# Optimization experiments

Hardware: AMD Instinct MI355X
Metric: run time of the kernel (lower is better)

Reference implementation:

```python
import jax, jax.numpy as jnp
import numpy as np

M, K1, N1, N2, N3 = 131072, 256, 1024, 1024, 256


def setup_inputs() -> dict:
    key = jax.random.key(0)
    k_x, k1, k2, k3 = jax.random.split(key, 4)
    x = jax.random.normal(k_x, (M, K1), dtype=jnp.float32)
    # Kaiming-ish scaling so softplus stays in a sane range
    w1 = jax.random.normal(k1, (K1, N1), dtype=jnp.float32) * (1.0 / np.sqrt(K1))
    w2 = jax.random.normal(k2, (N1, N2), dtype=jnp.float32) * (1.0 / np.sqrt(N1))
    w3 = jax.random.normal(k3, (N2, N3), dtype=jnp.float32) * (1.0 / np.sqrt(N2))
    return {"x": x, "w1": w1, "w2": w2, "w3": w3}


def reference(x, w1, w2, w3):
    # Fused 3-layer MLP: out = softplus(softplus(x @ W1) @ W2) @ W3
    h1 = jax.nn.softplus(x @ w1)   # [M, N1]
    h2 = jax.nn.softplus(h1 @ w2)  # [M, N2]
    return h2 @ w3                 # [M, N3]
```

## Files before the change

### kernel.cpp

```cpp
#include <hip/hip_runtime.h>

typedef __attribute__((ext_vector_type(8))) short short8;
typedef __attribute__((ext_vector_type(4))) float floatx4;
typedef __attribute__((ext_vector_type(2))) unsigned int uintx2;
typedef __attribute__((ext_vector_type(4))) unsigned int uintx4;
typedef unsigned short u16;

#define MFMA(a, b, c) __builtin_amdgcn_mfma_f32_16x16x32_bf16((a), (b), (c), 0, 0, 0)
#define BAR() do { asm volatile("" ::: "memory"); __builtin_amdgcn_s_barrier(); \
                   asm volatile("" ::: "memory"); } while (0)
#define LGKM0() asm volatile("s_waitcnt lgkmcnt(0)" ::: "memory")

__device__ __forceinline__ u16 f2bf(float f) {
  unsigned int u = __builtin_bit_cast(unsigned int, f);
  u += ((u >> 16) & 1u) + 0x7fffu;
  return (u16)(u >> 16);
}

__device__ __forceinline__ float softplus_f(float v) {
  float a = __builtin_fabsf(v);
  float e = __expf(-a);
  float l = __logf(1.0f + e);
  return __builtin_fmaxf(v, 0.0f) + l;
}

__device__ __forceinline__ unsigned int pack_sp(float lo, float hi) {
  return (unsigned int)f2bf(softplus_f(lo)) | ((unsigned int)f2bf(softplus_f(hi)) << 16);
}

__global__ void transpose_cvt(const float* __restrict__ in, u16* __restrict__ out, int K, int N) {
  __shared__ float tile[32][33];
  const int bn = blockIdx.x * 32, bk = blockIdx.y * 32;
  const int tx = threadIdx.x, ty = threadIdx.y;
#pragma unroll
  for (int i = 0; i < 32; i += 8)
    tile[ty + i][tx] = in[(size_t)(bk + ty + i) * N + bn + tx];
  __syncthreads();
#pragma unroll
  for (int i = 0; i < 32; i += 8)
    out[(size_t)(bn + ty + i) * K + bk + tx] = f2bf(tile[tx][ty + i]);
}

__device__ __forceinline__ void gld16(const void* g, void* l) {
  __builtin_amdgcn_global_load_lds((const __attribute__((address_space(1))) void*)g,
                                   (__attribute__((address_space(3))) void*)l, 16, 0, 0);
}

template <int LN>
__device__ __forceinline__ void vwait() {
  if constexpr (LN == 0) asm volatile("s_waitcnt vmcnt(0)" ::: "memory");
  else if constexpr (LN == 2) asm volatile("s_waitcnt vmcnt(2)" ::: "memory");
  else if constexpr (LN == 3) asm volatile("s_waitcnt vmcnt(3)" ::: "memory");
}

template <int K, int EPI, bool ACTF32>
__global__ __launch_bounds__(512, 4) void gemm2b(const void* __restrict__ actv,
                                                 const u16* __restrict__ wt,
                                                 void* __restrict__ Cout, int N, int nbn) {
  constexpr int H = K / 32;
  constexpr int BUF = 12288;
  __shared__ u16 lds[2 * BUF];
  u16* L = lds;
  const int tid = threadIdx.x, lane = tid & 63, wv = tid >> 6;
  const int l15 = lane & 15, g = lane >> 4;
  const int wvm = wv >> 2, wvn = wv & 3;
  const int nwg = gridDim.x, o = blockIdx.x;
  const int sw = (o & 7) * (nwg >> 3) + (o >> 3);
  const int bm = sw / nbn, bn = sw % nbn;
  const size_t am0 = (size_t)bm * 128;
  const size_t wn0 = (size_t)bn * 256;

  int afo[4], wfo[4];
#pragma unroll
  for (int mt = 0; mt < 4; ++mt) {
    const int r = wvm * 64 + mt * 16 + l15;
    afo[mt] = (r * 4 + (g ^ ((r >> 1) & 3))) * 8;
  }
#pragma unroll
  for (int nt = 0; nt < 4; ++nt) {
    const int r = wvn * 64 + nt * 16 + l15;
    wfo[nt] = 4096 + (r * 4 + (g ^ ((r >> 1) & 3))) * 8;
  }

  const int rA = tid >> 2, gA = (tid & 3) ^ ((rA >> 1) & 3);
  const int rW1 = 128 + rA, gW1 = (tid & 3) ^ ((rW1 >> 1) & 3);
  const u16* asrc = nullptr;
  const float* fsrc = nullptr;
  if constexpr (ACTF32) fsrc = (const float*)actv + (am0 + rA) * K + gA * 8;
  else asrc = (const u16*)actv + (am0 + rA) * K + gA * 8;
  const u16* wsrc0 = wt + (wn0 + rA) * K + gA * 8;
  const u16* wsrc1 = wt + (wn0 + rW1) * K + gW1 * 8;
  const int dA = tid * 8, dW0 = 4096 + tid * 8, dW1 = 4096 + (512 + tid) * 8;

#define STG_W(hh)                                                       \
  { gld16(wsrc0 + (hh) * 32, L + ((hh) & 1) * BUF + dW0);               \
    gld16(wsrc1 + (hh) * 32, L + ((hh) & 1) * BUF + dW1); }
#define STG_AB(hh) { gld16(asrc + (hh) * 32, L + ((hh) & 1) * BUF + dA); }
#define STG_AF(hh)                                                      \
  { floatx4 v0 = *(const floatx4*)(fsrc + (hh) * 32);                   \
    floatx4 v1 = *(const floatx4*)(fsrc + (hh) * 32 + 4);               \
    uintx4 w_;                                                          \
    w_.x = (unsigned)f2bf(v0.x) | ((unsigned)f2bf(v0.y) << 16);         \
    w_.y = (unsigned)f2bf(v0.z) | ((unsigned)f2bf(v0.w) << 16);         \
    w_.z = (unsigned)f2bf(v1.x) | ((unsigned)f2bf(v1.y) << 16);         \
    w_.w = (unsigned)f2bf(v1.z) | ((unsigned)f2bf(v1.w) << 16);         \
    *(uintx4*)(L + ((hh) & 1) * BUF + dA) = w_; }

  floatx4 acc[4][4];
  const floatx4 z4 = {0.f, 0.f, 0.f, 0.f};
#pragma unroll
  for (int nt = 0; nt < 4; ++nt)
#pragma unroll
    for (int mt = 0; mt < 4; ++mt) acc[nt][mt] = z4;

  if constexpr (ACTF32) { STG_AF(0) STG_W(0) }
  else { STG_AB(0) STG_W(0) }

#pragma unroll 1
  for (int h = 0; h < H; ++h) {
    const int cb = (h & 1) * BUF;
    if (h + 1 < H) {
      if constexpr (ACTF32) { STG_AF(h + 1) STG_W(h + 1) LGKM0(); vwait<2>(); }
      else { STG_AB(h + 1) STG_W(h + 1) vwait<3>(); }
    } else {
      if constexpr (ACTF32) LGKM0();
      vwait<0>();
    }
    BAR();
    short8 af0 = *(const short8*)(L + cb + afo[0]);
    short8 af1 = *(const short8*)(L + cb + afo[1]);
    short8 af2 = *(const short8*)(L + cb + afo[2]);
    short8 af3 = *(const short8*)(L + cb + afo[3]);
    short8 wf0 = *(const short8*)(L + cb + wfo[0]);
    short8 wf1 = *(const short8*)(L + cb + wfo[1]);
    short8 wf2 = *(const short8*)(L + cb + wfo[2]);
    short8 wf3 = *(const short8*)(L + cb + wfo[3]);
    __builtin_amdgcn_s_setprio(1);
    acc[0][0] = MFMA(wf0, af0, acc[0][0]);
    acc[0][1] = MFMA(wf0, af1, acc[0][1]);
    acc[0][2] = MFMA(wf0, af2, acc[0][2]);
    acc[0][3] = MFMA(wf0, af3, acc[0][3]);
    acc[1][0] = MFMA(wf1, af0, acc[1][0]);
    acc[1][1] = MFMA(wf1, af1, acc[1][1]);
    acc[1][2] = MFMA(wf1, af2, acc[1][2]);
    acc[1][3] = MFMA(wf1, af3, acc[1][3]);
    acc[2][0] = MFMA(wf2, af0, acc[2][0]);
    acc[2][1] = MFMA(wf2, af1, acc[2][1]);
    acc[2][2] = MFMA(wf2, af2, acc[2][2]);
    acc[2][3] = MFMA(wf2, af3, acc[2][3]);
    acc[3][0] = MFMA(wf3, af0, acc[3][0]);
    acc[3][1] = MFMA(wf3, af1, acc[3][1]);
    acc[3][2] = MFMA(wf3, af2, acc[3][2]);
    acc[3][3] = MFMA(wf3, af3, acc[3][3]);
    __builtin_amdgcn_s_setprio(0);
    BAR();
  }
#undef STG_W
#undef STG_AB
#undef STG_AF

  __syncthreads();

  if constexpr (EPI == 0) {
    u16* cl = L;
#pragma unroll
    for (int q = 0; q < 2; ++q) {
      if (q) __syncthreads();
      if (wvm == q) {
#pragma unroll
        for (int nt = 0; nt < 4; ++nt)
#pragma unroll
          for (int mt = 0; mt < 4; ++mt) {
            const int m = mt * 16 + l15;
            const int n0 = wvn * 64 + nt * 16 + g * 4;
            const int j = n0 >> 3, hh = (n0 >> 2) & 1;
            uintx2 pk;
            pk.x = pack_sp(acc[nt][mt].x, acc[nt][mt].y);
            pk.y = pack_sp(acc[nt][mt].z, acc[nt][mt].w);
            *(uintx2*)(cl + m * 256 + ((j ^ (m & 7)) << 3) + (hh << 2)) = pk;
          }
      }
      __syncthreads();
      u16* outp = (u16*)Cout;
#pragma unroll
      for (int i = 0; i < 4; ++i) {
        const int c = i * 512 + tid;
        const int m = c >> 5, j = c & 31;
        uintx4 v = *(const uintx4*)(cl + m * 256 + ((j ^ (m & 7)) << 3));
        *(uintx4*)(outp + (am0 + q * 64 + m) * N + wn0 + j * 8) = v;
      }
    }
  } else {
    float* cf = (float*)L;
#pragma unroll
    for (int q = 0; q < 4; ++q) {
      if (q) __syncthreads();
      if (wvm == (q >> 1)) {
#pragma unroll
        for (int nt = 0; nt < 4; ++nt)
#pragma unroll
          for (int mt2 = 0; mt2 < 2; ++mt2) {
            const int mt = (q & 1) * 2 + mt2;
            const int m = mt2 * 16 + l15;
            const int p = (wvn * 64 + nt * 16 + g * 4) >> 1;
            *(floatx4*)(cf + m * 256 + ((p ^ ((m & 7) << 1)) << 1)) = acc[nt][mt];
          }
      }
      __syncthreads();
      float* outp = (float*)Cout;
#pragma unroll
      for (int i = 0; i < 4; ++i) {
        const int c = i * 512 + tid;
        const int m = c >> 6, cc = c & 63;
        const int p = cc * 2;
        floatx4 v = *(const floatx4*)(cf + m * 256 + ((p ^ ((m & 7) << 1)) << 1));
        *(floatx4*)(outp + (am0 + q * 32 + m) * N + wn0 + cc * 4) = v;
      }
    }
  }
}

__global__ __launch_bounds__(512, 2) void mlp3_fused(const float* __restrict__ x,
                                                     const u16* __restrict__ w1t,
                                                     const u16* __restrict__ w2t,
                                                     const u16* __restrict__ w3t,
                                                     float* __restrict__ out) {
  __shared__ u16 h1s[64 * 1024];
  __shared__ u16 xs[64 * 256];
  const int tid = threadIdx.x, lane = tid & 63, wv = tid >> 6;
  const int l15 = lane & 15, g = lane >> 4;
  const size_t m0 = (size_t)blockIdx.x * 64;
  const floatx4 z4 = {0.f, 0.f, 0.f, 0.f};
  {
    const float* xp = x + m0 * 256;
#pragma unroll
    for (int r = 0; r < 8; ++r) {
      int idx4 = r * 512 + tid;
      int m = idx4 >> 6, k = (idx4 & 63) << 2;
      floatx4 v = *(const floatx4*)(xp + m * 256 + k);
      uintx2 pk;
      pk.x = (unsigned)f2bf(v.x) | ((unsigned)f2bf(v.y) << 16);
      pk.y = (unsigned)f2bf(v.z) | ((unsigned)f2bf(v.w) << 16);
      *(uintx2*)(xs + ((m * 256 + k) ^ ((m & 7) << 3))) = pk;
    }
  }
  __syncthreads();
#pragma unroll 1
  for (int c = 0; c < 4; ++c) {
    floatx4 acc[2][4];
#pragma unroll
    for (int t = 0; t < 2; ++t)
#pragma unroll
      for (int mt = 0; mt < 4; ++mt) acc[t][mt] = z4;
    const u16* p0 = w1t + (size_t)(c * 256 + wv * 32 + l15) * 256;
#pragma unroll
    for (int ks = 0; ks < 8; ++ks) {
      const int k = ks * 32 + g * 8;
      short8 a0 = *(const short8*)(p0 + k);
      short8 a1 = *(const short8*)(p0 + 16 * 256 + k);
      short8 b0 = *(const short8*)(xs + (((0 * 16 + l15) * 256 + k) ^ ((l15 & 7) << 3)));
      short8 b1 = *(const short8*)(xs + (((1 * 16 + l15) * 256 + k) ^ ((l15 & 7) << 3)));
      short8 b2 = *(const short8*)(xs + (((2 * 16 + l15) * 256 + k) ^ ((l15 & 7) << 3)));
      short8 b3 = *(const short8*)(xs + (((3 * 16 + l15) * 256 + k) ^ ((l15 & 7) << 3)));
      acc[0][0] = MFMA(a0, b0, acc[0][0]); acc[0][1] = MFMA(a0, b1, acc[0][1]);
      acc[0][2] = MFMA(a0, b2, acc[0][2]); acc[0][3] = MFMA(a0, b3, acc[0][3]);
      acc[1][0] = MFMA(a1, b0, acc[1][0]); acc[1][1] = MFMA(a1, b1, acc[1][1]);
      acc[1][2] = MFMA(a1, b2, acc[1][2]); acc[1][3] = MFMA(a1, b3, acc[1][3]);
    }
#pragma unroll
    for (int t = 0; t < 2; ++t)
#pragma unroll
      for (int mt = 0; mt < 4; ++mt) {
        const int n1 = c * 256 + wv * 32 + t * 16 + g * 4;
        const int m = mt * 16 + l15;
        uintx2 pk;
        pk.x = pack_sp(acc[t][mt].x, acc[t][mt].y);
        pk.y = pack_sp(acc[t][mt].z, acc[t][mt].w);
        *(uintx2*)(h1s + ((m * 1024 + n1) ^ ((m & 7) << 3))) = pk;
      }
  }
  __syncthreads();
  floatx4 acc3[2][4];
#pragma unroll
  for (int t = 0; t < 2; ++t)
#pragma unroll
    for (int mt = 0; mt < 4; ++mt) acc3[t][mt] = z4;
#pragma unroll 1
  for (int c2 = 0; c2 < 4; ++c2) {
    floatx4 acc2[2][4];
#pragma unroll
    for (int t = 0; t < 2; ++t)
#pragma unroll
      for (int mt = 0; mt < 4; ++mt) acc2[t][mt] = z4;
    {
      const u16* p0 = w2t + (size_t)(c2 * 256 + wv * 32 + l15) * 1024;
#pragma unroll 4
      for (int ks = 0; ks < 32; ++ks) {
        const int k = ks * 32 + g * 8;
        short8 a0 = *(const short8*)(p0 + k);
        short8 a1 = *(const short8*)(p0 + 16 * 1024 + k);
        short8 b0 = *(const short8*)(h1s + (((0 * 16 + l15) * 1024 + k) ^ ((l15 & 7) << 3)));
        short8 b1 = *(const short8*)(h1s + (((1 * 16 + l15) * 1024 + k) ^ ((l15 & 7) << 3)));
        short8 b2 = *(const short8*)(h1s + (((2 * 16 + l15) * 1024 + k) ^ ((l15 & 7) << 3)));
        short8 b3 = *(const short8*)(h1s + (((3 * 16 + l15) * 1024 + k) ^ ((l15 & 7) << 3)));
        acc2[0][0] = MFMA(a0, b0, acc2[0][0]); acc2[0][1] = MFMA(a0, b1, acc2[0][1]);
        acc2[0][2] = MFMA(a0, b2, acc2[0][2]); acc2[0][3] = MFMA(a0, b3, acc2[0][3]);
        acc2[1][0] = MFMA(a1, b0, acc2[1][0]); acc2[1][1] = MFMA(a1, b1, acc2[1][1]);
        acc2[1][2] = MFMA(a1, b2, acc2[1][2]); acc2[1][3] = MFMA(a1, b3, acc2[1][3]);
      }
    }
    __syncthreads();
#pragma unroll
    for (int t = 0; t < 2; ++t)
#pragma unroll
      for (int mt = 0; mt < 4; ++mt) {
        const int n2l = wv * 32 + t * 16 + g * 4;
        const int m = mt * 16 + l15;
        uintx2 pk;
        pk.x = pack_sp(acc2[t][mt].x, acc2[t][mt].y);
        pk.y = pack_sp(acc2[t][mt].z, acc2[t][mt].w);
        *(uintx2*)(xs + ((m * 256 + n2l) ^ ((m & 7) << 3))) = pk;
      }
    __syncthreads();
    {
      const u16* p0 = w3t + (size_t)(wv * 32 + l15) * 1024 + c2 * 256;
#pragma unroll
      for (int ks = 0; ks < 8; ++ks) {
        const int k = ks * 32 + g * 8;
        short8 a0 = *(const short8*)(p0 + k);
        short8 a1 = *(const short8*)(p0 + 16 * 1024 + k);
        short8 b0 = *(const short8*)(xs + (((0 * 16 + l15) * 256 + k) ^ ((l15 & 7) << 3)));
        short8 b1 = *(const short8*)(xs + (((1 * 16 + l15) * 256 + k) ^ ((l15 & 7) << 3)));
        short8 b2 = *(const short8*)(xs + (((2 * 16 + l15) * 256 + k) ^ ((l15 & 7) << 3)));
        short8 b3 = *(const short8*)(xs + (((3 * 16 + l15) * 256 + k) ^ ((l15 & 7) << 3)));
        acc3[0][0] = MFMA(a0, b0, acc3[0][0]); acc3[0][1] = MFMA(a0, b1, acc3[0][1]);
        acc3[0][2] = MFMA(a0, b2, acc3[0][2]); acc3[0][3] = MFMA(a0, b3, acc3[0][3]);
        acc3[1][0] = MFMA(a1, b0, acc3[1][0]); acc3[1][1] = MFMA(a1, b1, acc3[1][1]);
        acc3[1][2] = MFMA(a1, b2, acc3[1][2]); acc3[1][3] = MFMA(a1, b3, acc3[1][3]);
      }
    }
  }
#pragma unroll
  for (int t = 0; t < 2; ++t)
#pragma unroll
    for (int mt = 0; mt < 4; ++mt) {
      const int n3 = wv * 32 + t * 16 + g * 4;
      const int m = mt * 16 + l15;
      *(floatx4*)(out + (m0 + m) * 256 + n3) = acc3[t][mt];
    }
}

extern "C" void kernel_launch(void* const* d_in, const int* in_sizes, int n_in,
                              void* d_out, int out_size, void* d_ws, size_t ws_size,
                              hipStream_t stream) {
  const float* x = (const float*)d_in[0];
  const float* w1 = (const float*)d_in[1];
  const float* w2 = (const float*)d_in[2];
  const float* w3 = (const float*)d_in[3];
  float* out = (float*)d_out;
  const size_t M = 131072;

  u16* w1t = (u16*)d_ws;
  u16* w2t = w1t + 1024 * 256;
  u16* w3t = w2t + 1024 * 1024;
  u16* bufA = w3t + 256 * 1024;
  const size_t weights_el = 1024 * 256 + 1024 * 1024 + 256 * 1024;

  size_t CM = 0;
  const size_t cands[4] = {32768, 16384, 8192, 4096};
  for (int i = 0; i < 4; ++i) {
    size_t need = (weights_el + 2 * cands[i] * 1024) * sizeof(u16);
    if (ws_size >= need) { CM = cands[i]; break; }
  }

  dim3 tb(32, 8);
  transpose_cvt<<<dim3(32, 8), tb, 0, stream>>>(w1, w1t, 256, 1024);
  transpose_cvt<<<dim3(32, 32), tb, 0, stream>>>(w2, w2t, 1024, 1024);
  transpose_cvt<<<dim3(8, 32), tb, 0, stream>>>(w3, w3t, 1024, 256);

  if (CM) {
    u16* bufB = bufA + CM * 1024;
    const int nchunk = (int)(M / CM);
    for (int ci = 0; ci < nchunk; ++ci) {
      const float* xc = x + (size_t)ci * CM * 256;
      float* oc = out + (size_t)ci * CM * 256;
      gemm2b<256, 0, true><<<(int)(CM / 128) * 4, 512, 0, stream>>>(xc, w1t, bufA, 1024, 4);
      gemm2b<1024, 0, false><<<(int)(CM / 128) * 4, 512, 0, stream>>>(bufA, w2t, bufB, 1024, 4);
      gemm2b<1024, 1, false><<<(int)(CM / 128), 512, 0, stream>>>(bufB, w3t, oc, 256, 1);
    }
  } else {
    mlp3_fused<<<M / 64, 512, 0, stream>>>(x, w1t, w2t, w3t, out);
  }
}
```

Before: 661.9 us.

## Shrink GEMM tiles to 128x128 with 256-thread blocks and 4 waves

Each GEMM block changes from 128x256 with 8 waves to 128x128 with 4 waves, each wave still computing a 64x64 sub-tile. The staging loops, LDS buffer size, epilogue layout, grid sizes and vmcnt wait counts are adjusted to match. The intent is more, smaller blocks for better occupancy and load balance, with fewer epilogue passes through LDS. In exchange, each block reuses the weight and activation tiles across fewer outputs, so global and LDS traffic per FLOP goes up.

```diff
diff --git a/kernel.cpp b/kernel.cpp
--- a/kernel.cpp
+++ b/kernel.cpp
@@ -50,25 +50,25 @@
 __device__ __forceinline__ void vwait() {
   if constexpr (LN == 0) asm volatile("s_waitcnt vmcnt(0)" ::: "memory");
   else if constexpr (LN == 2) asm volatile("s_waitcnt vmcnt(2)" ::: "memory");
-  else if constexpr (LN == 3) asm volatile("s_waitcnt vmcnt(3)" ::: "memory");
+  else if constexpr (LN == 4) asm volatile("s_waitcnt vmcnt(4)" ::: "memory");
 }
 
 template <int K, int EPI, bool ACTF32>
-__global__ __launch_bounds__(512, 4) void gemm2b(const void* __restrict__ actv,
+__global__ __launch_bounds__(256, 3) void gemm97(const void* __restrict__ actv,
                                                  const u16* __restrict__ wt,
                                                  void* __restrict__ Cout, int N, int nbn) {
   constexpr int H = K / 32;
-  constexpr int BUF = 12288;
+  constexpr int BUF = 8192;
   __shared__ u16 lds[2 * BUF];
   u16* L = lds;
   const int tid = threadIdx.x, lane = tid & 63, wv = tid >> 6;
   const int l15 = lane & 15, g = lane >> 4;
-  const int wvm = wv >> 2, wvn = wv & 3;
+  const int wvm = wv >> 1, wvn = wv & 1;
   const int nwg = gridDim.x, o = blockIdx.x;
   const int sw = (o & 7) * (nwg >> 3) + (o >> 3);
   const int bm = sw / nbn, bn = sw % nbn;
   const size_t am0 = (size_t)bm * 128;
-  const size_t wn0 = (size_t)bn * 256;
+  const size_t wn0 = (size_t)bn * 128;
 
   int afo[4], wfo[4];
 #pragma unroll
@@ -82,29 +82,42 @@
     wfo[nt] = 4096 + (r * 4 + (g ^ ((r >> 1) & 3))) * 8;
   }
 
-  const int rA = tid >> 2, gA = (tid & 3) ^ ((rA >> 1) & 3);
-  const int rW1 = 128 + rA, gW1 = (tid & 3) ^ ((rW1 >> 1) & 3);
+  int rS[2], gS[2];
+#pragma unroll
+  for (int j = 0; j < 2; ++j) {
+    const int s = j * 256 + tid;
+    rS[j] = s >> 2;
+    gS[j] = (s & 3) ^ ((rS[j] >> 1) & 3);
+  }
   const u16* asrc = nullptr;
   const float* fsrc = nullptr;
-  if constexpr (ACTF32) fsrc = (const float*)actv + (am0 + rA) * K + gA * 8;
-  else asrc = (const u16*)actv + (am0 + rA) * K + gA * 8;
-  const u16* wsrc0 = wt + (wn0 + rA) * K + gA * 8;
-  const u16* wsrc1 = wt + (wn0 + rW1) * K + gW1 * 8;
-  const int dA = tid * 8, dW0 = 4096 + tid * 8, dW1 = 4096 + (512 + tid) * 8;
-
-#define STG_W(hh)                                                       \
-  { gld16(wsrc0 + (hh) * 32, L + ((hh) & 1) * BUF + dW0);               \
-    gld16(wsrc1 + (hh) * 32, L + ((hh) & 1) * BUF + dW1); }
-#define STG_AB(hh) { gld16(asrc + (hh) * 32, L + ((hh) & 1) * BUF + dA); }
-#define STG_AF(hh)                                                      \
-  { floatx4 v0 = *(const floatx4*)(fsrc + (hh) * 32);                   \
-    floatx4 v1 = *(const floatx4*)(fsrc + (hh) * 32 + 4);               \
-    uintx4 w_;                                                          \
-    w_.x = (unsigned)f2bf(v0.x) | ((unsigned)f2bf(v0.y) << 16);         \
-    w_.y = (unsigned)f2bf(v0.z) | ((unsigned)f2bf(v0.w) << 16);         \
-    w_.z = (unsigned)f2bf(v1.x) | ((unsigned)f2bf(v1.y) << 16);         \
-    w_.w = (unsigned)f2bf(v1.z) | ((unsigned)f2bf(v1.w) << 16);         \
-    *(uintx4*)(L + ((hh) & 1) * BUF + dA) = w_; }
+  if constexpr (ACTF32) fsrc = (const float*)actv + am0 * K;
+  else asrc = (const u16*)actv + am0 * K;
+  const u16* wsrc = wt + wn0 * K;
+
+#define STG_W(hh)                                                                   \
+  { _Pragma("unroll") for (int j = 0; j < 2; ++j)                                   \
+      gld16(wsrc + (size_t)rS[j] * K + gS[j] * 8 + (hh) * 32,                       \
+            L + ((hh) & 1) * BUF + 4096 + (j * 256 + tid) * 8); }
+#define STG_AB(hh)                                                                  \
+  { _Pragma("unroll") for (int j = 0; j < 2; ++j)                                   \
+      gld16(asrc + (size_t)rS[j] * K + gS[j] * 8 + (hh) * 32,                       \
+            L + ((hh) & 1) * BUF + (j * 256 + tid) * 8); }
+#define STG_AF(hh)                                                                  \
+  { floatx4 v0[2], v1[2];                                                           \
+    _Pragma("unroll") for (int j = 0; j < 2; ++j) {                                 \
+      const float* p_ = fsrc + (size_t)rS[j] * K + gS[j] * 8 + (hh) * 32;           \
+      v0[j] = *(const floatx4*)p_;                                                  \
+      v1[j] = *(const floatx4*)(p_ + 4);                                            \
+    }                                                                               \
+    _Pragma("unroll") for (int j = 0; j < 2; ++j) {                                 \
+      uintx4 w_;                                                                    \
+      w_.x = (unsigned)f2bf(v0[j].x) | ((unsigned)f2bf(v0[j].y) << 16);             \
+      w_.y = (unsigned)f2bf(v0[j].z) | ((unsigned)f2bf(v0[j].w) << 16);             \
+      w_.z = (unsigned)f2bf(v1[j].x) | ((unsigned)f2bf(v1[j].y) << 16);             \
+      w_.w = (unsigned)f2bf(v1[j].z) | ((unsigned)f2bf(v1[j].w) << 16);             \
+      *(uintx4*)(L + ((hh) & 1) * BUF + (j * 256 + tid) * 8) = w_;                  \
+    } }
 
   floatx4 acc[4][4];
   const floatx4 z4 = {0.f, 0.f, 0.f, 0.f};
@@ -121,7 +134,7 @@
     const int cb = (h & 1) * BUF;
     if (h + 1 < H) {
       if constexpr (ACTF32) { STG_AF(h + 1) STG_W(h + 1) LGKM0(); vwait<2>(); }
-      else { STG_AB(h + 1) STG_W(h + 1) vwait<3>(); }
+      else { STG_AB(h + 1) STG_W(h + 1) vwait<4>(); }
     } else {
       if constexpr (ACTF32) LGKM0();
       vwait<0>();
@@ -164,6 +177,29 @@
   if constexpr (EPI == 0) {
     u16* cl = L;
 #pragma unroll
+    for (int nt = 0; nt < 4; ++nt)
+#pragma unroll
+      for (int mt = 0; mt < 4; ++mt) {
+        const int m = wvm * 64 + mt * 16 + l15;
+        const int n0 = wvn * 64 + nt * 16 + g * 4;
+        const int j = n0 >> 3, hh = (n0 >> 2) & 1;
+        uintx2 pk;
+        pk.x = pack_sp(acc[nt][mt].x, acc[nt][mt].y);
+        pk.y = pack_sp(acc[nt][mt].z, acc[nt][mt].w);
+        *(uintx2*)(cl + m * 128 + ((j ^ (m & 7)) << 3) + (hh << 2)) = pk;
+      }
+    __syncthreads();
+    u16* outp = (u16*)Cout;
+#pragma unroll
+    for (int i = 0; i < 8; ++i) {
+      const int c = i * 256 + tid;
+      const int m = c >> 4, j = c & 15;
+      uintx4 v = *(const uintx4*)(cl + m * 128 + ((j ^ (m & 7)) << 3));
+      *(uintx4*)(outp + (am0 + m) * N + wn0 + j * 8) = v;
+    }
+  } else {
+    float* cf = (float*)L;
+#pragma unroll
     for (int q = 0; q < 2; ++q) {
       if (q) __syncthreads();
       if (wvm == q) {
@@ -172,49 +208,19 @@
 #pragma unroll
           for (int mt = 0; mt < 4; ++mt) {
             const int m = mt * 16 + l15;
-            const int n0 = wvn * 64 + nt * 16 + g * 4;
-            const int j = n0 >> 3, hh = (n0 >> 2) & 1;
-            uintx2 pk;
-            pk.x = pack_sp(acc[nt][mt].x, acc[nt][mt].y);
-            pk.y = pack_sp(acc[nt][mt].z, acc[nt][mt].w);
-            *(uintx2*)(cl + m * 256 + ((j ^ (m & 7)) << 3) + (hh << 2)) = pk;
-          }
-      }
-      __syncthreads();
-      u16* outp = (u16*)Cout;
-#pragma unroll
-      for (int i = 0; i < 4; ++i) {
-        const int c = i * 512 + tid;
-        const int m = c >> 5, j = c & 31;
-        uintx4 v = *(const uintx4*)(cl + m * 256 + ((j ^ (m & 7)) << 3));
-        *(uintx4*)(outp + (am0 + q * 64 + m) * N + wn0 + j * 8) = v;
-      }
-    }
-  } else {
-    float* cf = (float*)L;
-#pragma unroll
-    for (int q = 0; q < 4; ++q) {
-      if (q) __syncthreads();
-      if (wvm == (q >> 1)) {
-#pragma unroll
-        for (int nt = 0; nt < 4; ++nt)
-#pragma unroll
-          for (int mt2 = 0; mt2 < 2; ++mt2) {
-            const int mt = (q & 1) * 2 + mt2;
-            const int m = mt2 * 16 + l15;
             const int p = (wvn * 64 + nt * 16 + g * 4) >> 1;
-            *(floatx4*)(cf + m * 256 + ((p ^ ((m & 7) << 1)) << 1)) = acc[nt][mt];
+            *(floatx4*)(cf + m * 128 + ((p ^ ((m & 7) << 1)) << 1)) = acc[nt][mt];
           }
       }
       __syncthreads();
       float* outp = (float*)Cout;
 #pragma unroll
-      for (int i = 0; i < 4; ++i) {
-        const int c = i * 512 + tid;
-        const int m = c >> 6, cc = c & 63;
+      for (int i = 0; i < 8; ++i) {
+        const int c = i * 256 + tid;
+        const int m = c >> 5, cc = c & 31;
         const int p = cc * 2;
-        floatx4 v = *(const floatx4*)(cf + m * 256 + ((p ^ ((m & 7) << 1)) << 1));
-        *(floatx4*)(outp + (am0 + q * 32 + m) * N + wn0 + cc * 4) = v;
+        floatx4 v = *(const floatx4*)(cf + m * 128 + ((p ^ ((m & 7) << 1)) << 1));
+        *(floatx4*)(outp + (am0 + q * 64 + m) * N + wn0 + cc * 4) = v;
       }
     }
   }
@@ -384,9 +390,9 @@
     for (int ci = 0; ci < nchunk; ++ci) {
       const float* xc = x + (size_t)ci * CM * 256;
       float* oc = out + (size_t)ci * CM * 256;
-      gemm2b<256, 0, true><<<(int)(CM / 128) * 4, 512, 0, stream>>>(xc, w1t, bufA, 1024, 4);
-      gemm2b<1024, 0, false><<<(int)(CM / 128) * 4, 512, 0, stream>>>(bufA, w2t, bufB, 1024, 4);
-      gemm2b<1024, 1, false><<<(int)(CM / 128), 512, 0, stream>>>(bufB, w3t, oc, 256, 1);
+      gemm97<256, 0, true><<<(int)(CM / 128) * 8, 256, 0, stream>>>(xc, w1t, bufA, 1024, 8);
+      gemm97<1024, 0, false><<<(int)(CM / 128) * 8, 256, 0, stream>>>(bufA, w2t, bufB, 1024, 8);
+      gemm97<1024, 1, false><<<(int)(CM / 128) * 2, 256, 0, stream>>>(bufB, w3t, oc, 256, 2);
     }
   } else {
     mlp3_fused<<<M / 64, 512, 0, stream>>>(x, w1t, w2t, w3t, out);
```

Result: no change. 657.6 us (-0.6%).
